# Kernel optimization log

Hardware: AMD Instinct MI355X
Metric: run time of the kernel (lower is better)

## Reference

```python
import jax, jax.numpy as jnp
import numpy as np

IRR_IN = 4
IRR_OUT = 4
N_SCALAR = 64
E = 1_000_000
DIM = IRR_IN * IRR_OUT * 2  # 32
HID = 2 * DIM               # 64

# ir_1: swap-pair gather index [1,0,3,2,5,4,7,6]
IR_1 = np.concatenate([np.array([1, 0]) + 2 * i for i in range(IRR_IN)])
# ir_2: alternating sign [1,-1,1,-1,...]
IR_2 = np.ones(2 * IRR_IN, dtype=np.float32)
IR_2[1::2] = -1.0


def setup_inputs() -> dict:
    key = jax.random.key(0)
    ks = jax.random.split(key, 4)
    x = jax.random.normal(ks[0], (E, IRR_IN, 2), dtype=jnp.float32)
    s = jax.random.normal(ks[1], (E, N_SCALAR), dtype=jnp.float32)
    W1 = jax.random.normal(ks[2], (N_SCALAR, HID), dtype=jnp.float32) * (1.0 / np.sqrt(N_SCALAR))
    b1 = jnp.zeros((HID,), dtype=jnp.float32)
    W2 = jax.random.normal(ks[3], (HID, DIM), dtype=jnp.float32) * (1.0 / np.sqrt(HID))
    b2 = jnp.zeros((DIM,), dtype=jnp.float32)
    return {"x": x, "s": s, "W1": W1, "b1": b1, "W2": W2, "b2": b2}


def reference(x, s, W1, b1, W2, b2):
    ir1 = jnp.asarray(IR_1)
    ir2 = jnp.asarray(IR_2)
    # per-edge MLP producing raw weights: [E, irr_out, 2*irr_in]
    h = jax.nn.relu(s @ W1 + b1)
    w = (h @ W2 + b2).reshape(-1, IRR_OUT, 2 * IRR_IN)
    w_1 = w[:, :, ir1]        # pair-swapped copy
    w_2 = w * ir2             # sign-alternated copy
    # stack -> [E, 2, irr_out, 2*irr_in]; permute -> [E, 2*irr_in, irr_out, 2]
    wm = jnp.stack((w_2, w_1), axis=1).transpose(0, 3, 2, 1)
    wm = wm.reshape(-1, 2 * IRR_IN, 2 * IRR_OUT)  # [E, 2*irr_in, 2*irr_out]
    xf = x.reshape(-1, 2 * IRR_IN)                # [E, 2*irr_in]
    out = jnp.einsum('ei,eio->eo', xf, wm)        # tiny per-edge matvec
    return out.reshape(-1, IRR_OUT, 2)
```

## Files before the change

### kernel.cpp

```cpp
#include <hip/hip_runtime.h>
#include <hip/hip_bf16.h>

typedef __bf16 bf16x8 __attribute__((ext_vector_type(8)));
typedef __bf16 bf16x4 __attribute__((ext_vector_type(4)));
typedef float  f32x4  __attribute__((ext_vector_type(4)));
typedef float  f32x2  __attribute__((ext_vector_type(2)));

__global__ __launch_bounds__(256) void so2_fused_kernel(
    const float* __restrict__ x, const float* __restrict__ s,
    const float* __restrict__ W1, const float* __restrict__ b1v,
    const float* __restrict__ W2, const float* __restrict__ b2v,
    float* __restrict__ out, int E)
{
  __shared__ unsigned short lds_w1t[64 * 64];
  __shared__ unsigned short lds_w2t[32 * 64];
  __shared__ char lds_h[4][8192];

  const int tid  = threadIdx.x;
  const int wid  = tid >> 6;
  const int lane = tid & 63;
  const int lrow = lane & 15;
  const int lg   = lane >> 4;

  const int web = blockIdx.x * 256 + wid * 64;
  const bool wave_active = (web < E);
  const int base_e = wave_active ? web : 0;

  f32x4 sv[4][4];
  #pragma unroll
  for (int et = 0; et < 4; ++et) {
    int er = base_e + et * 16 + lrow; er = er < E ? er : E - 1;
    const float* sp = s + (size_t)er * 64 + lg * 8;
    sv[et][0] = *(const f32x4*)(sp);
    sv[et][1] = *(const f32x4*)(sp + 4);
    sv[et][2] = *(const f32x4*)(sp + 32);
    sv[et][3] = *(const f32x4*)(sp + 36);
  }
  f32x4 xv[4];
  #pragma unroll
  for (int et = 0; et < 4; ++et) {
    int er = base_e + et * 16 + lrow; er = er < E ? er : E - 1;
    xv[et] = *(const f32x4*)(x + (size_t)er * 8 + (lg & 1) * 4);
  }
  f32x4 bias1[4], bias2[2];
  #pragma unroll
  for (int jt = 0; jt < 4; ++jt) bias1[jt] = *(const f32x4*)(b1v + jt * 16 + lg * 4);
  #pragma unroll
  for (int dt = 0; dt < 2; ++dt) bias2[dt] = *(const f32x4*)(b2v + dt * 16 + lg * 4);

  #pragma unroll
  for (int it = 0; it < 4; ++it) {
    int i = (it * 256 + tid) * 4;
    f32x4 v = *(const f32x4*)(W1 + i);
    int k = i >> 6, j = i & 63;
    #pragma unroll
    for (int q = 0; q < 4; ++q) {
      int byte = ((j + q) << 7) + (k << 1);
      byte ^= ((j + q) & 7) << 4;
      *(unsigned short*)((char*)lds_w1t + byte) =
          __builtin_bit_cast(unsigned short, (__bf16)v[q]);
    }
  }
  #pragma unroll
  for (int it = 0; it < 2; ++it) {
    int i = (it * 256 + tid) * 4;
    f32x4 v = *(const f32x4*)(W2 + i);
    int k = i >> 5, d = i & 31;
    #pragma unroll
    for (int q = 0; q < 4; ++q) {
      int byte = ((d + q) << 7) + (k << 1);
      byte ^= ((d + q) & 7) << 4;
      *(unsigned short*)((char*)lds_w2t + byte) =
          __builtin_bit_cast(unsigned short, (__bf16)v[q]);
    }
  }

  bf16x8 sf[4][2];
  #pragma unroll
  for (int et = 0; et < 4; ++et) {
    #pragma unroll
    for (int c = 0; c < 2; ++c) {
      #pragma unroll
      for (int i = 0; i < 4; ++i) {
        sf[et][c][i]     = (__bf16)sv[et][c * 2][i];
        sf[et][c][i + 4] = (__bf16)sv[et][c * 2 + 1][i];
      }
    }
  }

  __syncthreads();
  if (!wave_active) return;

  char* hbuf = lds_h[wid];

  #pragma unroll
  for (int jt = 0; jt < 4; ++jt) {
    bf16x8 wf[2];
    #pragma unroll
    for (int c = 0; c < 2; ++c) {
      int j = jt * 16 + lrow;
      int byte = (j << 7) + ((c * 32 + lg * 8) << 1);
      byte ^= (j & 7) << 4;
      wf[c] = *(const bf16x8*)((const char*)lds_w1t + byte);
    }
    #pragma unroll
    for (int et = 0; et < 4; ++et) {
      f32x4 acc = bias1[jt];
      acc = __builtin_amdgcn_mfma_f32_16x16x32_bf16(wf[0], sf[et][0], acc, 0, 0, 0);
      acc = __builtin_amdgcn_mfma_f32_16x16x32_bf16(wf[1], sf[et][1], acc, 0, 0, 0);
      bf16x4 hv;
      #pragma unroll
      for (int r = 0; r < 4; ++r) hv[r] = (__bf16)fmaxf(acc[r], 0.f);
      int byte = ((et * 16 + lrow) << 7) + ((jt * 16 + lg * 4) << 1);
      byte ^= (lrow & 7) << 4;
      *(bf16x4*)(hbuf + byte) = hv;
    }
  }

  asm volatile("s_waitcnt lgkmcnt(0)" ::: "memory");
  __builtin_amdgcn_sched_barrier(0);

  bf16x8 w2f[2][2];
  #pragma unroll
  for (int dt = 0; dt < 2; ++dt) {
    #pragma unroll
    for (int c = 0; c < 2; ++c) {
      int d = dt * 16 + lrow;
      int byte = (d << 7) + ((c * 32 + lg * 8) << 1);
      byte ^= (d & 7) << 4;
      w2f[dt][c] = *(const bf16x8*)((const char*)lds_w2t + byte);
    }
  }
  f32x4 wacc[4][2];
  #pragma unroll
  for (int et = 0; et < 4; ++et) {
    bf16x8 hf[2];
    #pragma unroll
    for (int c = 0; c < 2; ++c) {
      int byte = ((et * 16 + lrow) << 7) + ((c * 32 + lg * 8) << 1);
      byte ^= (lrow & 7) << 4;
      hf[c] = *(const bf16x8*)(hbuf + byte);
    }
    #pragma unroll
    for (int dt = 0; dt < 2; ++dt) {
      f32x4 acc = bias2[dt];
      acc = __builtin_amdgcn_mfma_f32_16x16x32_bf16(w2f[dt][0], hf[0], acc, 0, 0, 0);
      acc = __builtin_amdgcn_mfma_f32_16x16x32_bf16(w2f[dt][1], hf[1], acc, 0, 0, 0);
      wacc[et][dt] = acc;
    }
  }

  #pragma unroll
  for (int et = 0; et < 4; ++et) {
    f32x4 xe = xv[et];
    float qr[2], qi[2];
    #pragma unroll
    for (int dt = 0; dt < 2; ++dt) {
      f32x4 a = wacc[et][dt];
      float pr = xe[0] * a[0] - xe[1] * a[1] + xe[2] * a[2] - xe[3] * a[3];
      float pi = xe[0] * a[1] + xe[1] * a[0] + xe[2] * a[3] + xe[3] * a[2];
      qr[dt] = pr + __shfl_xor(pr, 16, 64);
      qi[dt] = pi + __shfl_xor(pi, 16, 64);
    }
    const int sel = lg & 1;
    const int o = (lg >> 1) + 2 * sel;
    const float vr = sel ? qr[1] : qr[0];
    const float vi = sel ? qi[1] : qi[0];
    const int e = web + et * 16 + lrow;
    if (e < E) {
      f32x2 v2 = {vr, vi};
      *(f32x2*)(out + (size_t)e * 8 + o * 2) = v2;
    }
  }
}

extern "C" void kernel_launch(void* const* d_in, const int* in_sizes, int n_in,
                              void* d_out, int out_size, void* d_ws, size_t ws_size,
                              hipStream_t stream) {
  const float* x  = (const float*)d_in[0];
  const float* s  = (const float*)d_in[1];
  const float* W1 = (const float*)d_in[2];
  const float* b1 = (const float*)d_in[3];
  const float* W2 = (const float*)d_in[4];
  const float* b2 = (const float*)d_in[5];
  float* out = (float*)d_out;
  const int E = in_sizes[0] / 8;
  const int blocks = (E + 255) / 256;
  so2_fused_kernel<<<blocks, 256, 0, stream>>>(x, s, W1, b1, W2, b2, out, E);
}
```

Measured before the change: 68.29 us.

## Make fused SO2 kernel persistent and software-pipeline edge halves

Launches at most 1024 blocks that loop over 256-edge chunks, so the weight transpose and staging into LDS is paid once per block instead of once per chunk. Each wave processes its 64 edges as two 32-edge halves, issuing the second half's s loads before the first half's second GEMM to overlap memory latency with MFMA work. This halves the per-wave h buffer and adds full/partial templated paths to skip bounds clamps. Fewer blocks may reduce latency hiding if occupancy per CU is insufficient.

```diff
diff --git a/kernel.cpp b/kernel.cpp
--- a/kernel.cpp
+++ b/kernel.cpp
@@ -6,7 +6,119 @@
 typedef float  f32x4  __attribute__((ext_vector_type(4)));
 typedef float  f32x2  __attribute__((ext_vector_type(2)));
 
-__global__ __launch_bounds__(256) void so2_fused_kernel(
+#define MFMA16(A, B, C) __builtin_amdgcn_mfma_f32_16x16x32_bf16(A, B, C, 0, 0, 0)
+#define FENCE_WAIT() do { asm volatile("s_waitcnt lgkmcnt(0)" ::: "memory"); \
+                          __builtin_amdgcn_sched_barrier(0); } while (0)
+
+template <bool FULL>
+__device__ __forceinline__ void load_pair_s(const float* __restrict__ s, int ebase,
+                                            int lrow, int lg, int E, bf16x8 sf[2][2])
+{
+  #pragma unroll
+  for (int q = 0; q < 2; ++q) {
+    int er = ebase + q * 16 + lrow;
+    if (!FULL) er = er < E ? er : E - 1;
+    const float* sp = s + (size_t)er * 64 + lg * 8;
+    f32x4 a0 = *(const f32x4*)(sp);
+    f32x4 a1 = *(const f32x4*)(sp + 4);
+    f32x4 a2 = *(const f32x4*)(sp + 32);
+    f32x4 a3 = *(const f32x4*)(sp + 36);
+    #pragma unroll
+    for (int i = 0; i < 4; ++i) {
+      sf[q][0][i] = (__bf16)a0[i]; sf[q][0][i + 4] = (__bf16)a1[i];
+      sf[q][1][i] = (__bf16)a2[i]; sf[q][1][i + 4] = (__bf16)a3[i];
+    }
+  }
+}
+
+__device__ __forceinline__ void gemm1_to_lds(char* hbuf, const unsigned short* w1t,
+                                             const bf16x8 sf[2][2], const f32x4 bias1[4],
+                                             int lrow, int lg)
+{
+  #pragma unroll
+  for (int jt = 0; jt < 4; ++jt) {
+    const int j = jt * 16 + lrow;
+    int wb0 = (j << 7) + ((lg * 8) << 1);      wb0 ^= (j & 7) << 4;
+    int wb1 = (j << 7) + ((32 + lg * 8) << 1); wb1 ^= (j & 7) << 4;
+    bf16x8 wf0 = *(const bf16x8*)((const char*)w1t + wb0);
+    bf16x8 wf1 = *(const bf16x8*)((const char*)w1t + wb1);
+    #pragma unroll
+    for (int q = 0; q < 2; ++q) {
+      f32x4 acc = bias1[jt];
+      acc = MFMA16(wf0, sf[q][0], acc);
+      acc = MFMA16(wf1, sf[q][1], acc);
+      bf16x4 hv;
+      #pragma unroll
+      for (int r = 0; r < 4; ++r) hv[r] = (__bf16)fmaxf(acc[r], 0.f);
+      int byte = ((q * 16 + lrow) << 7) + ((jt * 16 + lg * 4) << 1);
+      byte ^= (lrow & 7) << 4;
+      *(bf16x4*)(hbuf + byte) = hv;
+    }
+  }
+}
+
+template <bool FULL>
+__device__ __forceinline__ void gemm2_epilogue(const char* hbuf, const unsigned short* w2t,
+                                               const float* __restrict__ x,
+                                               const f32x4 bias2[2],
+                                               float* __restrict__ out,
+                                               int ebase, int lrow, int lg, int E)
+{
+  f32x4 xv[2];
+  #pragma unroll
+  for (int q = 0; q < 2; ++q) {
+    int er = ebase + q * 16 + lrow;
+    if (!FULL) er = er < E ? er : E - 1;
+    xv[q] = *(const f32x4*)(x + (size_t)er * 8 + (lg & 1) * 4);
+  }
+  bf16x8 hf[2][2];
+  #pragma unroll
+  for (int q = 0; q < 2; ++q)
+    #pragma unroll
+    for (int c = 0; c < 2; ++c) {
+      int byte = ((q * 16 + lrow) << 7) + ((c * 32 + lg * 8) << 1);
+      byte ^= (lrow & 7) << 4;
+      hf[q][c] = *(const bf16x8*)(hbuf + byte);
+    }
+  bf16x8 w2f[2][2];
+  #pragma unroll
+  for (int dt = 0; dt < 2; ++dt)
+    #pragma unroll
+    for (int c = 0; c < 2; ++c) {
+      int d = dt * 16 + lrow;
+      int byte = (d << 7) + ((c * 32 + lg * 8) << 1);
+      byte ^= (d & 7) << 4;
+      w2f[dt][c] = *(const bf16x8*)((const char*)w2t + byte);
+    }
+  __builtin_amdgcn_sched_barrier(0);
+
+  #pragma unroll
+  for (int q = 0; q < 2; ++q) {
+    f32x4 xe = xv[q];
+    float qr[2], qi[2];
+    #pragma unroll
+    for (int dt = 0; dt < 2; ++dt) {
+      f32x4 a = bias2[dt];
+      a = MFMA16(w2f[dt][0], hf[q][0], a);
+      a = MFMA16(w2f[dt][1], hf[q][1], a);
+      float pr = xe[0] * a[0] - xe[1] * a[1] + xe[2] * a[2] - xe[3] * a[3];
+      float pi = xe[0] * a[1] + xe[1] * a[0] + xe[2] * a[3] + xe[3] * a[2];
+      qr[dt] = pr + __shfl_xor(pr, 16, 64);
+      qi[dt] = pi + __shfl_xor(pi, 16, 64);
+    }
+    const int sel = lg & 1;
+    const int o = (lg >> 1) + 2 * sel;
+    const float vr = sel ? qr[1] : qr[0];
+    const float vi = sel ? qi[1] : qi[0];
+    const int e = ebase + q * 16 + lrow;
+    if (FULL || e < E) {
+      f32x2 v2 = {vr, vi};
+      *(f32x2*)(out + (size_t)e * 8 + o * 2) = v2;
+    }
+  }
+}
+
+__global__ __launch_bounds__(256, 4) void so2_fused_kernel(
     const float* __restrict__ x, const float* __restrict__ s,
     const float* __restrict__ W1, const float* __restrict__ b1v,
     const float* __restrict__ W2, const float* __restrict__ b2v,
@@ -14,7 +126,7 @@
 {
   __shared__ unsigned short lds_w1t[64 * 64];
   __shared__ unsigned short lds_w2t[32 * 64];
-  __shared__ char lds_h[4][8192];
+  __shared__ char lds_h[4][4096];
 
   const int tid  = threadIdx.x;
   const int wid  = tid >> 6;
@@ -22,32 +134,6 @@
   const int lrow = lane & 15;
   const int lg   = lane >> 4;
 
-  const int web = blockIdx.x * 256 + wid * 64;
-  const bool wave_active = (web < E);
-  const int base_e = wave_active ? web : 0;
-
-  f32x4 sv[4][4];
-  #pragma unroll
-  for (int et = 0; et < 4; ++et) {
-    int er = base_e + et * 16 + lrow; er = er < E ? er : E - 1;
-    const float* sp = s + (size_t)er * 64 + lg * 8;
-    sv[et][0] = *(const f32x4*)(sp);
-    sv[et][1] = *(const f32x4*)(sp + 4);
-    sv[et][2] = *(const f32x4*)(sp + 32);
-    sv[et][3] = *(const f32x4*)(sp + 36);
-  }
-  f32x4 xv[4];
-  #pragma unroll
-  for (int et = 0; et < 4; ++et) {
-    int er = base_e + et * 16 + lrow; er = er < E ? er : E - 1;
-    xv[et] = *(const f32x4*)(x + (size_t)er * 8 + (lg & 1) * 4);
-  }
-  f32x4 bias1[4], bias2[2];
-  #pragma unroll
-  for (int jt = 0; jt < 4; ++jt) bias1[jt] = *(const f32x4*)(b1v + jt * 16 + lg * 4);
-  #pragma unroll
-  for (int dt = 0; dt < 2; ++dt) bias2[dt] = *(const f32x4*)(b2v + dt * 16 + lg * 4);
-
   #pragma unroll
   for (int it = 0; it < 4; ++it) {
     int i = (it * 256 + tid) * 4;
@@ -74,102 +160,39 @@
           __builtin_bit_cast(unsigned short, (__bf16)v[q]);
     }
   }
-
-  bf16x8 sf[4][2];
-  #pragma unroll
-  for (int et = 0; et < 4; ++et) {
-    #pragma unroll
-    for (int c = 0; c < 2; ++c) {
-      #pragma unroll
-      for (int i = 0; i < 4; ++i) {
-        sf[et][c][i]     = (__bf16)sv[et][c * 2][i];
-        sf[et][c][i + 4] = (__bf16)sv[et][c * 2 + 1][i];
-      }
-    }
-  }
-
+  f32x4 bias1[4], bias2[2];
+  #pragma unroll
+  for (int jt = 0; jt < 4; ++jt) bias1[jt] = *(const f32x4*)(b1v + jt * 16 + lg * 4);
+  #pragma unroll
+  for (int dt = 0; dt < 2; ++dt) bias2[dt] = *(const f32x4*)(b2v + dt * 16 + lg * 4);
   __syncthreads();
-  if (!wave_active) return;
 
   char* hbuf = lds_h[wid];
-
-  #pragma unroll
-  for (int jt = 0; jt < 4; ++jt) {
-    bf16x8 wf[2];
-    #pragma unroll
-    for (int c = 0; c < 2; ++c) {
-      int j = jt * 16 + lrow;
-      int byte = (j << 7) + ((c * 32 + lg * 8) << 1);
-      byte ^= (j & 7) << 4;
-      wf[c] = *(const bf16x8*)((const char*)lds_w1t + byte);
-    }
-    #pragma unroll
-    for (int et = 0; et < 4; ++et) {
-      f32x4 acc = bias1[jt];
-      acc = __builtin_amdgcn_mfma_f32_16x16x32_bf16(wf[0], sf[et][0], acc, 0, 0, 0);
-      acc = __builtin_amdgcn_mfma_f32_16x16x32_bf16(wf[1], sf[et][1], acc, 0, 0, 0);
-      bf16x4 hv;
-      #pragma unroll
-      for (int r = 0; r < 4; ++r) hv[r] = (__bf16)fmaxf(acc[r], 0.f);
-      int byte = ((et * 16 + lrow) << 7) + ((jt * 16 + lg * 4) << 1);
-      byte ^= (lrow & 7) << 4;
-      *(bf16x4*)(hbuf + byte) = hv;
-    }
-  }
-
-  asm volatile("s_waitcnt lgkmcnt(0)" ::: "memory");
-  __builtin_amdgcn_sched_barrier(0);
-
-  bf16x8 w2f[2][2];
-  #pragma unroll
-  for (int dt = 0; dt < 2; ++dt) {
-    #pragma unroll
-    for (int c = 0; c < 2; ++c) {
-      int d = dt * 16 + lrow;
-      int byte = (d << 7) + ((c * 32 + lg * 8) << 1);
-      byte ^= (d & 7) << 4;
-      w2f[dt][c] = *(const bf16x8*)((const char*)lds_w2t + byte);
-    }
-  }
-  f32x4 wacc[4][2];
-  #pragma unroll
-  for (int et = 0; et < 4; ++et) {
-    bf16x8 hf[2];
-    #pragma unroll
-    for (int c = 0; c < 2; ++c) {
-      int byte = ((et * 16 + lrow) << 7) + ((c * 32 + lg * 8) << 1);
-      byte ^= (lrow & 7) << 4;
-      hf[c] = *(const bf16x8*)(hbuf + byte);
-    }
-    #pragma unroll
-    for (int dt = 0; dt < 2; ++dt) {
-      f32x4 acc = bias2[dt];
-      acc = __builtin_amdgcn_mfma_f32_16x16x32_bf16(w2f[dt][0], hf[0], acc, 0, 0, 0);
-      acc = __builtin_amdgcn_mfma_f32_16x16x32_bf16(w2f[dt][1], hf[1], acc, 0, 0, 0);
-      wacc[et][dt] = acc;
-    }
-  }
-
-  #pragma unroll
-  for (int et = 0; et < 4; ++et) {
-    f32x4 xe = xv[et];
-    float qr[2], qi[2];
-    #pragma unroll
-    for (int dt = 0; dt < 2; ++dt) {
-      f32x4 a = wacc[et][dt];
-      float pr = xe[0] * a[0] - xe[1] * a[1] + xe[2] * a[2] - xe[3] * a[3];
-      float pi = xe[0] * a[1] + xe[1] * a[0] + xe[2] * a[3] + xe[3] * a[2];
-      qr[dt] = pr + __shfl_xor(pr, 16, 64);
-      qi[dt] = pi + __shfl_xor(pi, 16, 64);
-    }
-    const int sel = lg & 1;
-    const int o = (lg >> 1) + 2 * sel;
-    const float vr = sel ? qr[1] : qr[0];
-    const float vi = sel ? qi[1] : qi[0];
-    const int e = web + et * 16 + lrow;
-    if (e < E) {
-      f32x2 v2 = {vr, vi};
-      *(f32x2*)(out + (size_t)e * 8 + o * 2) = v2;
+  const int nChunks = (E + 255) >> 8;
+
+  for (int c = blockIdx.x; c < nChunks; c += gridDim.x) {
+    const int web = c * 256 + wid * 64;
+    if (web >= E) continue;
+    if (web + 64 <= E) {
+      bf16x8 sf0[2][2], sf1[2][2];
+      load_pair_s<true>(s, web, lrow, lg, E, sf0);
+      gemm1_to_lds(hbuf, lds_w1t, sf0, bias1, lrow, lg);
+      load_pair_s<true>(s, web + 32, lrow, lg, E, sf1);
+      FENCE_WAIT();
+      gemm2_epilogue<true>(hbuf, lds_w2t, x, bias2, out, web, lrow, lg, E);
+      gemm1_to_lds(hbuf, lds_w1t, sf1, bias1, lrow, lg);
+      FENCE_WAIT();
+      gemm2_epilogue<true>(hbuf, lds_w2t, x, bias2, out, web + 32, lrow, lg, E);
+    } else {
+      bf16x8 sf0[2][2], sf1[2][2];
+      load_pair_s<false>(s, web, lrow, lg, E, sf0);
+      gemm1_to_lds(hbuf, lds_w1t, sf0, bias1, lrow, lg);
+      load_pair_s<false>(s, web + 32, lrow, lg, E, sf1);
+      FENCE_WAIT();
+      gemm2_epilogue<false>(hbuf, lds_w2t, x, bias2, out, web, lrow, lg, E);
+      gemm1_to_lds(hbuf, lds_w1t, sf1, bias1, lrow, lg);
+      FENCE_WAIT();
+      gemm2_epilogue<false>(hbuf, lds_w2t, x, bias2, out, web + 32, lrow, lg, E);
     }
   }
 }
@@ -185,6 +208,7 @@
   const float* b2 = (const float*)d_in[5];
   float* out = (float*)d_out;
   const int E = in_sizes[0] / 8;
-  const int blocks = (E + 255) / 256;
+  const int nChunks = (E + 255) / 256;
+  const int blocks = nChunks < 1024 ? nChunks : 1024;
   so2_fused_kernel<<<blocks, 256, 0, stream>>>(x, s, W1, b1, W2, b2, out, E);
 }
```

After: 71.34 us. +4.5%, slower.

## Loop each wave over 16-edge tiles with register prefetch of next tile

Applied to the files above, without the earlier changes.

Each block now covers 1024 edges, and each wave loops over sixteen 16-edge tiles instead of processing 64 edges at once. The s and x rows for the next tile are prefetched into registers while the current tile's two MFMA layers run. This spreads the cost of converting and staging W1/W2 into LDS over four times as many edges and lowers register and LDS use per wave (h buffer 2KB, launch bounds 256,4), which should allow higher occupancy. The trade-off is four times fewer blocks and a serial per-tile dependency chain with an LDS wait between the layers, so there is less memory-level parallelism per wave.

```diff
diff --git a/kernel.cpp b/kernel.cpp
--- a/kernel.cpp
+++ b/kernel.cpp
@@ -6,7 +6,12 @@
 typedef float  f32x4  __attribute__((ext_vector_type(4)));
 typedef float  f32x2  __attribute__((ext_vector_type(2)));
 
-__global__ __launch_bounds__(256) void so2_fused_kernel(
+#define MFMA16(A, B, C) __builtin_amdgcn_mfma_f32_16x16x32_bf16(A, B, C, 0, 0, 0)
+#define FENCE_WAIT() do { asm volatile("s_waitcnt lgkmcnt(0)" ::: "memory"); \
+                          __builtin_amdgcn_sched_barrier(0); } while (0)
+#define FENCE_COMPILER() asm volatile("" ::: "memory")
+
+__global__ __launch_bounds__(256, 4) void so2_fused_kernel(
     const float* __restrict__ x, const float* __restrict__ s,
     const float* __restrict__ W1, const float* __restrict__ b1v,
     const float* __restrict__ W2, const float* __restrict__ b2v,
@@ -14,7 +19,7 @@
 {
   __shared__ unsigned short lds_w1t[64 * 64];
   __shared__ unsigned short lds_w2t[32 * 64];
-  __shared__ char lds_h[4][8192];
+  __shared__ char lds_h[4][2048];
 
   const int tid  = threadIdx.x;
   const int wid  = tid >> 6;
@@ -22,26 +27,6 @@
   const int lrow = lane & 15;
   const int lg   = lane >> 4;
 
-  const int web = blockIdx.x * 256 + wid * 64;
-  const bool wave_active = (web < E);
-  const int base_e = wave_active ? web : 0;
-
-  f32x4 sv[4][4];
-  #pragma unroll
-  for (int et = 0; et < 4; ++et) {
-    int er = base_e + et * 16 + lrow; er = er < E ? er : E - 1;
-    const float* sp = s + (size_t)er * 64 + lg * 8;
-    sv[et][0] = *(const f32x4*)(sp);
-    sv[et][1] = *(const f32x4*)(sp + 4);
-    sv[et][2] = *(const f32x4*)(sp + 32);
-    sv[et][3] = *(const f32x4*)(sp + 36);
-  }
-  f32x4 xv[4];
-  #pragma unroll
-  for (int et = 0; et < 4; ++et) {
-    int er = base_e + et * 16 + lrow; er = er < E ? er : E - 1;
-    xv[et] = *(const f32x4*)(x + (size_t)er * 8 + (lg & 1) * 4);
-  }
   f32x4 bias1[4], bias2[2];
   #pragma unroll
   for (int jt = 0; jt < 4; ++jt) bias1[jt] = *(const f32x4*)(b1v + jt * 16 + lg * 4);
@@ -74,55 +59,11 @@
           __builtin_bit_cast(unsigned short, (__bf16)v[q]);
     }
   }
-
-  bf16x8 sf[4][2];
-  #pragma unroll
-  for (int et = 0; et < 4; ++et) {
-    #pragma unroll
-    for (int c = 0; c < 2; ++c) {
-      #pragma unroll
-      for (int i = 0; i < 4; ++i) {
-        sf[et][c][i]     = (__bf16)sv[et][c * 2][i];
-        sf[et][c][i + 4] = (__bf16)sv[et][c * 2 + 1][i];
-      }
-    }
-  }
-
   __syncthreads();
-  if (!wave_active) return;
-
-  char* hbuf = lds_h[wid];
-
-  #pragma unroll
-  for (int jt = 0; jt < 4; ++jt) {
-    bf16x8 wf[2];
-    #pragma unroll
-    for (int c = 0; c < 2; ++c) {
-      int j = jt * 16 + lrow;
-      int byte = (j << 7) + ((c * 32 + lg * 8) << 1);
-      byte ^= (j & 7) << 4;
-      wf[c] = *(const bf16x8*)((const char*)lds_w1t + byte);
-    }
-    #pragma unroll
-    for (int et = 0; et < 4; ++et) {
-      f32x4 acc = bias1[jt];
-      acc = __builtin_amdgcn_mfma_f32_16x16x32_bf16(wf[0], sf[et][0], acc, 0, 0, 0);
-      acc = __builtin_amdgcn_mfma_f32_16x16x32_bf16(wf[1], sf[et][1], acc, 0, 0, 0);
-      bf16x4 hv;
-      #pragma unroll
-      for (int r = 0; r < 4; ++r) hv[r] = (__bf16)fmaxf(acc[r], 0.f);
-      int byte = ((et * 16 + lrow) << 7) + ((jt * 16 + lg * 4) << 1);
-      byte ^= (lrow & 7) << 4;
-      *(bf16x4*)(hbuf + byte) = hv;
-    }
-  }
-
-  asm volatile("s_waitcnt lgkmcnt(0)" ::: "memory");
-  __builtin_amdgcn_sched_barrier(0);
 
   bf16x8 w2f[2][2];
   #pragma unroll
-  for (int dt = 0; dt < 2; ++dt) {
+  for (int dt = 0; dt < 2; ++dt)
     #pragma unroll
     for (int c = 0; c < 2; ++c) {
       int d = dt * 16 + lrow;
@@ -130,33 +71,82 @@
       byte ^= (d & 7) << 4;
       w2f[dt][c] = *(const bf16x8*)((const char*)lds_w2t + byte);
     }
-  }
-  f32x4 wacc[4][2];
-  #pragma unroll
-  for (int et = 0; et < 4; ++et) {
-    bf16x8 hf[2];
-    #pragma unroll
-    for (int c = 0; c < 2; ++c) {
-      int byte = ((et * 16 + lrow) << 7) + ((c * 32 + lg * 8) << 1);
-      byte ^= (lrow & 7) << 4;
-      hf[c] = *(const bf16x8*)(hbuf + byte);
-    }
-    #pragma unroll
-    for (int dt = 0; dt < 2; ++dt) {
-      f32x4 acc = bias2[dt];
-      acc = __builtin_amdgcn_mfma_f32_16x16x32_bf16(w2f[dt][0], hf[0], acc, 0, 0, 0);
-      acc = __builtin_amdgcn_mfma_f32_16x16x32_bf16(w2f[dt][1], hf[1], acc, 0, 0, 0);
-      wacc[et][dt] = acc;
-    }
+
+  const int wbase = blockIdx.x * 1024 + wid * 256;
+  const int rem = E - wbase;
+  const int nt = rem <= 0 ? 0 : (rem >= 256 ? 16 : ((rem + 15) >> 4));
+  if (nt == 0) return;
+
+  char* hbuf = lds_h[wid];
+
+  f32x4 sN[4];
+  f32x4 xN;
+  {
+    int er = wbase + lrow; er = er < E ? er : E - 1;
+    const float* sp = s + (size_t)er * 64 + lg * 8;
+    sN[0] = *(const f32x4*)(sp);
+    sN[1] = *(const f32x4*)(sp + 4);
+    sN[2] = *(const f32x4*)(sp + 32);
+    sN[3] = *(const f32x4*)(sp + 36);
+    xN = *(const f32x4*)(x + (size_t)er * 8 + (lg & 1) * 4);
   }
 
-  #pragma unroll
-  for (int et = 0; et < 4; ++et) {
-    f32x4 xe = xv[et];
+  for (int t = 0; t < nt; ++t) {
+    const int ebase = wbase + t * 16;
+
+    bf16x8 sf0, sf1;
+    #pragma unroll
+    for (int i = 0; i < 4; ++i) {
+      sf0[i] = (__bf16)sN[0][i]; sf0[i + 4] = (__bf16)sN[1][i];
+      sf1[i] = (__bf16)sN[2][i]; sf1[i + 4] = (__bf16)sN[3][i];
+    }
+    const f32x4 xe = xN;
+
+    {
+      int er = ebase + 16 + lrow; er = er < E ? er : E - 1;
+      const float* sp = s + (size_t)er * 64 + lg * 8;
+      sN[0] = *(const f32x4*)(sp);
+      sN[1] = *(const f32x4*)(sp + 4);
+      sN[2] = *(const f32x4*)(sp + 32);
+      sN[3] = *(const f32x4*)(sp + 36);
+      xN = *(const f32x4*)(x + (size_t)er * 8 + (lg & 1) * 4);
+    }
+
+    #pragma unroll
+    for (int jt = 0; jt < 4; ++jt) {
+      const int j = jt * 16 + lrow;
+      int wb0 = (j << 7) + ((lg * 8) << 1);      wb0 ^= (j & 7) << 4;
+      int wb1 = (j << 7) + ((32 + lg * 8) << 1); wb1 ^= (j & 7) << 4;
+      bf16x8 wf0 = *(const bf16x8*)((const char*)lds_w1t + wb0);
+      bf16x8 wf1 = *(const bf16x8*)((const char*)lds_w1t + wb1);
+      f32x4 acc = bias1[jt];
+      acc = MFMA16(wf0, sf0, acc);
+      acc = MFMA16(wf1, sf1, acc);
+      bf16x4 hv;
+      #pragma unroll
+      for (int r = 0; r < 4; ++r) hv[r] = (__bf16)fmaxf(acc[r], 0.f);
+      int byte = (lrow << 7) + ((jt * 16 + lg * 4) << 1);
+      byte ^= (lrow & 7) << 4;
+      *(bf16x4*)(hbuf + byte) = hv;
+    }
+
+    FENCE_WAIT();
+
+    bf16x8 hf0, hf1;
+    {
+      int b0 = (lrow << 7) + ((lg * 8) << 1);      b0 ^= (lrow & 7) << 4;
+      int b1 = (lrow << 7) + ((32 + lg * 8) << 1); b1 ^= (lrow & 7) << 4;
+      hf0 = *(const bf16x8*)(hbuf + b0);
+      hf1 = *(const bf16x8*)(hbuf + b1);
+    }
+    FENCE_COMPILER();
+
     float qr[2], qi[2];
     #pragma unroll
     for (int dt = 0; dt < 2; ++dt) {
-      f32x4 a = wacc[et][dt];
+      f32x4 a = bias2[dt];
+      a = MFMA16(w2f[dt][0], hf0, a);
+      a = MFMA16(w2f[dt][1], hf1, a);
       float pr = xe[0] * a[0] - xe[1] * a[1] + xe[2] * a[2] - xe[3] * a[3];
       float pi = xe[0] * a[1] + xe[1] * a[0] + xe[2] * a[3] + xe[3] * a[2];
       qr[dt] = pr + __shfl_xor(pr, 16, 64);
@@ -166,7 +156,7 @@
     const int o = (lg >> 1) + 2 * sel;
     const float vr = sel ? qr[1] : qr[0];
     const float vi = sel ? qi[1] : qi[0];
-    const int e = web + et * 16 + lrow;
+    const int e = ebase + lrow;
     if (e < E) {
       f32x2 v2 = {vr, vi};
       *(f32x2*)(out + (size_t)e * 8 + o * 2) = v2;
@@ -185,6 +175,6 @@
   const float* b2 = (const float*)d_in[5];
   float* out = (float*)d_out;
   const int E = in_sizes[0] / 8;
-  const int blocks = (E + 255) / 256;
+  const int blocks = (E + 1023) / 1024;
   so2_fused_kernel<<<blocks, 256, 0, stream>>>(x, s, W1, b1, W2, b2, out, E);
 }
```

After: 64.97 us. -4.9%, faster.
